# Performance work log

Hardware: AMD Instinct MI355X
Metric: run time of the kernel (lower is better)

## Reference

```python
import jax, jax.numpy as jnp
import numpy as np
from jax import lax

B, L, D, F, K = 16, 1024, 384, 1536, 3
MAX_DUR = 10          # clamp on per-token duration (makes output length static)
T_OUT = L * MAX_DUR   # padded expanded length
ALPHA = 1.0
EPS = 1e-5


def conv1d_same(x_ncl, w, b):
    # x_ncl: [B, Cin, L], w: [Cout, Cin, K]
    y = lax.conv_general_dilated(x_ncl, w, window_strides=(1,), padding='SAME',
                                 dimension_numbers=('NCH', 'OIH', 'NCH'))
    return y + b[None, :, None]


def conv_block(x, wA, bA, wB, bB):
    # x: [B, L, D] -> Conv(D->F) ReLU Conv(F->D) ReLU -> [B, L, D]
    h = x.transpose(0, 2, 1)
    h = jax.nn.relu(conv1d_same(h, wA, bA))
    h = jax.nn.relu(conv1d_same(h, wB, bB))
    return h.transpose(0, 2, 1)


def layernorm(x, g, b):
    mu = jnp.mean(x, axis=-1, keepdims=True)
    var = jnp.var(x, axis=-1, keepdims=True)
    return (x - mu) * lax.rsqrt(var + EPS) * g + b


def setup_inputs() -> dict:
    key = jax.random.key(0)
    ks = jax.random.split(key, 8)
    s = 0.02
    return {
        'y': jax.random.normal(ks[0], (B, L, D), jnp.float32),
        'token_lengths': jax.random.randint(ks[1], (B,), 1, L + 1).astype(jnp.int32),
        'w1a': jax.random.normal(ks[2], (F, D, K), jnp.float32) * s,
        'b1a': jnp.zeros((F,), jnp.float32),
        'w1b': jax.random.normal(ks[3], (D, F, K), jnp.float32) * s,
        'b1b': jnp.zeros((D,), jnp.float32),
        'g1': jnp.ones((D,), jnp.float32),
        'be1': jnp.zeros((D,), jnp.float32),
        'w2a': jax.random.normal(ks[4], (F, D, K), jnp.float32) * s,
        'b2a': jnp.zeros((F,), jnp.float32),
        'w2b': jax.random.normal(ks[5], (D, F, K), jnp.float32) * s,
        'b2b': jnp.zeros((D,), jnp.float32),
        'g2': jnp.ones((D,), jnp.float32),
        'be2': jnp.zeros((D,), jnp.float32),
        'wl': jax.random.normal(ks[6], (D, 1), jnp.float32) * s,
        'bl': jnp.zeros((1,), jnp.float32),
    }


def reference(y, token_lengths, w1a, b1a, w1b, b1b, g1, be1,
              w2a, b2a, w2b, b2b, g2, be2, wl, bl):
    # DurationPredictor (eval mode: dropout is identity)
    h = conv_block(y, w1a, b1a, w1b, b1b)
    h = layernorm(h, g1, be1)
    h = conv_block(h, w2a, b2a, w2b, b2b)
    h = layernorm(h, g2, be2)
    preds = h @ wl + bl                      # [B, L, 1]

    # lengths = round(alpha * exp(preds)), masked to valid tokens, clamped
    lns = jnp.round(ALPHA * jnp.exp(preds[..., 0]))
    lns = jnp.clip(lns, 0, MAX_DUR).astype(jnp.int32)        # [B, L]
    mask = jnp.arange(L)[None, :] < token_lengths[:, None]
    lns = jnp.where(mask, lns, 0)

    # ragged repeat_interleave + pad, fully vectorized:
    # output frame t maps to token idx = searchsorted(cumsum(lns), t, 'right')
    csum = jnp.cumsum(lns, axis=1)                            # [B, L]
    totals = csum[:, -1]                                      # [B]
    t = jnp.arange(T_OUT, dtype=jnp.int32)
    idx = jax.vmap(lambda c: jnp.searchsorted(c, t, side='right'))(csum)  # [B, T_OUT]
    idx = jnp.minimum(idx, L - 1)
    gathered = jnp.take_along_axis(y, idx[..., None], axis=1)  # [B, T_OUT, D]
    valid = t[None, :] < totals[:, None]
    enlarged = jnp.where(valid[..., None], gathered, 0.0)
    return enlarged, totals
```

## Files before the change

### kernel.cpp

```cpp
#include <hip/hip_runtime.h>
#include <hip/hip_bf16.h>

#define BB 16
#define LL 1024
#define DD 384
#define FF 1536
#define KK 3
#define T_OUT 10240
#define MAX_DUR 10

#define PADL 1026
#define LO_SCALE 2048.0f
#define LO_INV   4.8828125e-4f

typedef _Float16 f16x8 __attribute__((ext_vector_type(8)));
typedef float    f32x4 __attribute__((ext_vector_type(4)));

__device__ __forceinline__ void gll16(const void* g, void* l) {
    __builtin_amdgcn_global_load_lds(
        (const __attribute__((address_space(1))) void*)g,
        (__attribute__((address_space(3))) void*)l, 16, 0, 0);
}

__device__ __forceinline__ void split_write(float v, _Float16* hi, _Float16* lo, size_t off) {
    _Float16 h = (_Float16)v;
    hi[off] = h;
    lo[off] = (_Float16)((v - (float)h) * LO_SCALE);
}

__device__ __forceinline__ float split_read(const _Float16* hi, const _Float16* lo, size_t off) {
    return (float)hi[off] + (float)lo[off] * LO_INV;
}

__global__ void wfrag_k(const float* __restrict__ w, _Float16* __restrict__ hi,
                        _Float16* __restrict__ lo, int O, int I) {
    int id = blockIdx.x * 256 + threadIdx.x;
    int total = O * 3 * I;
    if (id >= total) return;
    int e = id & 7;
    int lane = (id >> 3) & 63;
    int rest = id >> 9;
    int nKT = (3 * I) >> 5;
    int ktl = rest % nKT;
    int ot = rest / nKT;
    int o = ot * 16 + (lane & 15);
    int koff = ((lane >> 4) << 3) + e;
    int kseg = ktl % 3;
    int i = (ktl / 3) * 32 + koff;
    float v = w[(o * I + i) * 3 + kseg];
    split_write(v, hi, lo, id);
}

__global__ void ysplit_k(const float* __restrict__ y, _Float16* __restrict__ hi,
                         _Float16* __restrict__ lo) {
    int id = blockIdx.x * 256 + threadIdx.x;
    if (id >= BB * PADL * DD) return;
    int d = id % DD;
    int r = id / DD;
    int b = r / PADL;
    int lr = r - b * PADL;
    float v = 0.f;
    if (lr >= 1 && lr <= LL) v = y[((size_t)(b << 10) + (lr - 1)) * DD + d];
    split_write(v, hi, lo, id);
}

__global__ void padzero_k(_Float16* __restrict__ hi, _Float16* __restrict__ lo, int width) {
    int id = blockIdx.x * 256 + threadIdx.x;
    if (id >= BB * 2 * width) return;
    int b = id / (2 * width);
    int rem = id - b * 2 * width;
    int row = (rem / width) ? (PADL - 1) : 0;
    int c = rem % width;
    size_t off = (size_t)(b * PADL + row) * width + c;
    hi[off] = (_Float16)0.f;
    lo[off] = (_Float16)0.f;
}

__global__ __launch_bounds__(256, 2) void gemm_split(
        const _Float16* __restrict__ Ahi, const _Float16* __restrict__ Alo,
        const _Float16* __restrict__ WfH, const _Float16* __restrict__ WfL,
        const float* __restrict__ bias,
        _Float16* __restrict__ Ohi, _Float16* __restrict__ Olo,
        int Cin, int Cout, int Ktot, int nN) {
    __shared__ _Float16 lds_h[16384];
    const int tid = threadIdx.x;
    const int lane = tid & 63;
    const int w = tid >> 6;
    const int lm = lane & 15, lq = lane >> 4;
    const int xcd = blockIdx.x & 7;
    const int t2 = blockIdx.x >> 3;
    const int g  = t2 / (4 * nN);
    const int r  = t2 - g * (4 * nN);
    const int n_t = r >> 2;
    const int mi  = r & 3;
    const int m_t = ((g * 4 + mi) << 3) + xcd;
    const int m0 = m_t << 7;
    const int n0 = n_t << 7;
    const int b = m0 >> 10;
    const int l0 = m0 & 1023;
    const int rowBase = b * PADL + l0;
    const int wm = (w >> 1) * 64, wn = (w & 1) * 64;

    f32x4 accM[4][4], accC[4][4];
    const f32x4 zz = {0.f, 0.f, 0.f, 0.f};
    #pragma unroll
    for (int i = 0; i < 4; ++i)
        #pragma unroll
        for (int jj = 0; jj < 4; ++jj) { accM[i][jj] = zz; accC[i][jj] = zz; }

    const int nKT = Ktot >> 5;

    auto stageA = [&](int kt, int nxt) {
        int kseg = kt % 3;
        int d0 = (kt / 3) << 5;
        #pragma unroll
        for (int it = 0; it < 2; ++it) {
            int s = (w * 2 + it) * 64 + lane;
            int p = s >> 3, sl = s & 7;
            int t = sl ^ (p & 7);
            int m = p * 2 + (t >> 2);
            int k8 = t & 3;
            size_t aoff = (size_t)(rowBase + m + kseg) * Cin + d0 + k8 * 8;
            _Float16* lbase = lds_h + nxt * 8192 + (size_t)(w * 2 + it) * 512;
            gll16(Ahi + aoff, lbase);
            gll16(Alo + aoff, lbase + 4096);
        }
    };

    auto loadB = [&](int kt, f16x8* bH, f16x8* bL) {
        int ktc = kt < nKT ? kt : nKT - 1;
        #pragma unroll
        for (int jj = 0; jj < 4; ++jj) {
            int ntg = (n0 + wn + jj * 16) >> 4;
            size_t boff = (((size_t)ntg * nKT + ktc) * 64 + lane) * 8;
            bH[jj] = *(const f16x8*)(WfH + boff);
            bL[jj] = *(const f16x8*)(WfL + boff);
        }
    };

    auto compute = [&](const _Float16* lb, const f16x8* bH, const f16x8* bL) {
        #pragma unroll
        for (int i = 0; i < 4; ++i) {
            int m = wm + i * 16 + lm;
            int p = m >> 1;
            int sl = (((m & 1) << 2) | lq) ^ (p & 7);
            int off = p * 64 + sl * 8;
            f16x8 aH = *(const f16x8*)(lb + off);
            f16x8 aL = *(const f16x8*)(lb + 4096 + off);
            #pragma unroll
            for (int jj = 0; jj < 4; ++jj) {
                accM[i][jj] = __builtin_amdgcn_mfma_f32_16x16x32_f16(aH, bH[jj], accM[i][jj], 0, 0, 0);
                accC[i][jj] = __builtin_amdgcn_mfma_f32_16x16x32_f16(aH, bL[jj], accC[i][jj], 0, 0, 0);
                accC[i][jj] = __builtin_amdgcn_mfma_f32_16x16x32_f16(aL, bH[jj], accC[i][jj], 0, 0, 0);
            }
        }
    };

    f16x8 b0H[4], b0L[4], b1H[4], b1L[4];
    loadB(0, b0H, b0L);
    stageA(0, 0);
    for (int kt = 0; kt < nKT; kt += 2) {
        __syncthreads();
        loadB(kt + 1, b1H, b1L);
        if (kt + 1 < nKT) stageA(kt + 1, 1);
        compute(lds_h, b0H, b0L);
        __syncthreads();
        loadB(kt + 2, b0H, b0L);
        if (kt + 2 < nKT) stageA(kt + 2, 0);
        if (kt + 1 < nKT) compute(lds_h + 8192, b1H, b1L);
    }
    #pragma unroll
    for (int i = 0; i < 4; ++i)
        #pragma unroll
        for (int jj = 0; jj < 4; ++jj) {
            int n_g = n0 + wn + jj * 16 + lm;
            float bv = bias[n_g];
            #pragma unroll
            for (int rr = 0; rr < 4; ++rr) {
                int l = l0 + wm + i * 16 + lq * 4 + rr;
                float v = accM[i][jj][rr] + accC[i][jj][rr] * LO_INV + bv;
                v = fmaxf(v, 0.f);
                size_t off = (size_t)(b * PADL + 1 + l) * Cout + n_g;
                split_write(v, Ohi, Olo, off);
            }
        }
}

__global__ __launch_bounds__(128) void ln_split_k(
        _Float16* __restrict__ hi, _Float16* __restrict__ lo,
        const float* __restrict__ g, const float* __restrict__ be) {
    const int row = blockIdx.x;
    const int b = row >> 10, l = row & 1023;
    const size_t base = (size_t)(b * PADL + 1 + l) * DD;
    const int tid = threadIdx.x;
    float v0 = split_read(hi, lo, base + tid);
    float v1 = split_read(hi, lo, base + tid + 128);
    float v2 = split_read(hi, lo, base + tid + 256);

    __shared__ float sh[2];
    float s = v0 + v1 + v2;
    #pragma unroll
    for (int o = 32; o > 0; o >>= 1) s += __shfl_down(s, o, 64);
    if ((tid & 63) == 0) sh[tid >> 6] = s;
    __syncthreads();
    float mu = (sh[0] + sh[1]) * (1.f / DD);
    __syncthreads();
    float d0 = v0 - mu, d1 = v1 - mu, d2 = v2 - mu;
    float q = d0 * d0 + d1 * d1 + d2 * d2;
    #pragma unroll
    for (int o = 32; o > 0; o >>= 1) q += __shfl_down(q, o, 64);
    if ((tid & 63) == 0) sh[tid >> 6] = q;
    __syncthreads();
    float var = (sh[0] + sh[1]) * (1.f / DD);
    float rs = rsqrtf(var + 1e-5f);
    split_write(d0 * rs * g[tid] + be[tid], hi, lo, base + tid);
    split_write(d1 * rs * g[tid + 128] + be[tid + 128], hi, lo, base + tid + 128);
    split_write(d2 * rs * g[tid + 256] + be[tid + 256], hi, lo, base + tid + 256);
}

__global__ __launch_bounds__(128) void ln_pred_split_k(
        const _Float16* __restrict__ hi, const _Float16* __restrict__ lo,
        const float* __restrict__ g, const float* __restrict__ be,
        const float* __restrict__ wl, const float* __restrict__ bl,
        const int* __restrict__ token_lengths, int* __restrict__ lns) {
    const int row = blockIdx.x;
    const int b = row >> 10, l = row & 1023;
    const size_t base = (size_t)(b * PADL + 1 + l) * DD;
    const int tid = threadIdx.x;
    float v0 = split_read(hi, lo, base + tid);
    float v1 = split_read(hi, lo, base + tid + 128);
    float v2 = split_read(hi, lo, base + tid + 256);

    __shared__ float sh[2];
    float s = v0 + v1 + v2;
    #pragma unroll
    for (int o = 32; o > 0; o >>= 1) s += __shfl_down(s, o, 64);
    if ((tid & 63) == 0) sh[tid >> 6] = s;
    __syncthreads();
    float mu = (sh[0] + sh[1]) * (1.f / DD);
    __syncthreads();
    float d0 = v0 - mu, d1 = v1 - mu, d2 = v2 - mu;
    float q = d0 * d0 + d1 * d1 + d2 * d2;
    #pragma unroll
    for (int o = 32; o > 0; o >>= 1) q += __shfl_down(q, o, 64);
    if ((tid & 63) == 0) sh[tid >> 6] = q;
    __syncthreads();
    float var = (sh[0] + sh[1]) * (1.f / DD);
    float rs = rsqrtf(var + 1e-5f);
    __syncthreads();
    float p = (d0 * rs * g[tid]       + be[tid])       * wl[tid]
            + (d1 * rs * g[tid + 128] + be[tid + 128]) * wl[tid + 128]
            + (d2 * rs * g[tid + 256] + be[tid + 256]) * wl[tid + 256];
    #pragma unroll
    for (int o = 32; o > 0; o >>= 1) p += __shfl_down(p, o, 64);
    if ((tid & 63) == 0) sh[tid >> 6] = p;
    __syncthreads();
    if (tid == 0) {
        float pred = sh[0] + sh[1] + bl[0];
        float e = expf(pred);
        float r = rintf(e);
        r = fminf(fmaxf(r, 0.f), (float)MAX_DUR);
        int v = (int)r;
        if (l >= token_lengths[b]) v = 0;
        lns[row] = v;
    }
}

__global__ __launch_bounds__(1024) void cumsum_k(
        const int* __restrict__ lns, int* __restrict__ csum,
        float* __restrict__ totals_out) {
    __shared__ int s[1024];
    const int b = blockIdx.x, tid = threadIdx.x;
    s[tid] = lns[(b << 10) + tid];
    __syncthreads();
    #pragma unroll
    for (int o = 1; o < 1024; o <<= 1) {
        int t = (tid >= o) ? s[tid - o] : 0;
        __syncthreads();
        s[tid] += t;
        __syncthreads();
    }
    csum[(b << 10) + tid] = s[tid];
    if (tid == 1023) totals_out[b] = (float)s[1023];
}

__global__ __launch_bounds__(256) void gather_k(
        const float* __restrict__ y, const int* __restrict__ csum,
        float* __restrict__ out) {
    int gid = blockIdx.x * 256 + threadIdx.x;
    int c4 = gid % 96;
    int rest = gid / 96;
    int t = rest % T_OUT;
    int b = rest / T_OUT;
    const int* c = csum + (b << 10);
    int total = c[1023];
    float4 r = make_float4(0.f, 0.f, 0.f, 0.f);
    if (t < total) {
        int lo = 0, hi = 1024;
        while (lo < hi) {
            int mid = (lo + hi) >> 1;
            if (c[mid] <= t) lo = mid + 1; else hi = mid;
        }
        int idx = min(lo, LL - 1);
        r = *(const float4*)(y + ((size_t)((b << 10) + idx)) * DD + (c4 << 2));
    }
    *(float4*)(out + ((size_t)b * T_OUT + t) * DD + (c4 << 2)) = r;
}

extern "C" void kernel_launch(void* const* d_in, const int* in_sizes, int n_in,
                              void* d_out, int out_size, void* d_ws, size_t ws_size,
                              hipStream_t stream) {
    const float* y   = (const float*)d_in[0];
    const int*   tok = (const int*)d_in[1];
    const float* w1a = (const float*)d_in[2];
    const float* b1a = (const float*)d_in[3];
    const float* w1b = (const float*)d_in[4];
    const float* b1b = (const float*)d_in[5];
    const float* g1  = (const float*)d_in[6];
    const float* be1 = (const float*)d_in[7];
    const float* w2a = (const float*)d_in[8];
    const float* b2a = (const float*)d_in[9];
    const float* w2b = (const float*)d_in[10];
    const float* b2b = (const float*)d_in[11];
    const float* g2  = (const float*)d_in[12];
    const float* be2 = (const float*)d_in[13];
    const float* wl  = (const float*)d_in[14];
    const float* bl  = (const float*)d_in[15];

    float* out = (float*)d_out;

    const size_t WN   = (size_t)FF * DD * KK;
    const size_t SN   = (size_t)BB * PADL * DD;
    const size_t H1N  = (size_t)BB * PADL * FF;
    _Float16* p = (_Float16*)d_ws;
    _Float16* Wh1a = p;              _Float16* Wl1a = Wh1a + WN;
    _Float16* Wh1b = Wl1a + WN;      _Float16* Wl1b = Wh1b + WN;
    _Float16* Wh2a = Wl1b + WN;      _Float16* Wl2a = Wh2a + WN;
    _Float16* Wh2b = Wl2a + WN;      _Float16* Wl2b = Wh2b + WN;
    _Float16* Shi  = Wl2b + WN;      _Float16* Slo  = Shi + SN;
    _Float16* H1hi = Slo + SN;       _Float16* H1lo = H1hi + H1N;
    int* lns  = (int*)(H1lo + H1N);
    int* csum = lns + BB * LL;

    const int M = BB * LL;

    {
        int n = FF * DD * KK;
        wfrag_k<<<(n + 255) / 256, 256, 0, stream>>>(w1a, Wh1a, Wl1a, FF, DD);
        wfrag_k<<<(n + 255) / 256, 256, 0, stream>>>(w1b, Wh1b, Wl1b, DD, FF);
        wfrag_k<<<(n + 255) / 256, 256, 0, stream>>>(w2a, Wh2a, Wl2a, FF, DD);
        wfrag_k<<<(n + 255) / 256, 256, 0, stream>>>(w2b, Wh2b, Wl2b, DD, FF);
        int ny = BB * PADL * DD;
        ysplit_k<<<(ny + 255) / 256, 256, 0, stream>>>(y, Shi, Slo);
        int np = BB * 2 * FF;
        padzero_k<<<(np + 255) / 256, 256, 0, stream>>>(H1hi, H1lo, FF);
    }
    gemm_split<<<(FF / 128) * (M / 128), 256, 0, stream>>>(Shi, Slo, Wh1a, Wl1a, b1a, H1hi, H1lo, DD, FF, 3 * DD, FF / 128);
    gemm_split<<<(DD / 128) * (M / 128), 256, 0, stream>>>(H1hi, H1lo, Wh1b, Wl1b, b1b, Shi, Slo, FF, DD, 3 * FF, DD / 128);
    ln_split_k<<<M, 128, 0, stream>>>(Shi, Slo, g1, be1);
    gemm_split<<<(FF / 128) * (M / 128), 256, 0, stream>>>(Shi, Slo, Wh2a, Wl2a, b2a, H1hi, H1lo, DD, FF, 3 * DD, FF / 128);
    gemm_split<<<(DD / 128) * (M / 128), 256, 0, stream>>>(H1hi, H1lo, Wh2b, Wl2b, b2b, Shi, Slo, FF, DD, 3 * FF, DD / 128);
    ln_pred_split_k<<<M, 128, 0, stream>>>(Shi, Slo, g2, be2, wl, bl, tok, lns);
    cumsum_k<<<BB, 1024, 0, stream>>>(lns, csum, out + (size_t)BB * T_OUT * DD);
    {
        long long n = (long long)BB * T_OUT * 96;
        gather_k<<<(int)((n + 255) / 256), 256, 0, stream>>>(y, csum, out);
    }
}
```

Measured before the change: 1.072 ms.

## Quad-buffer GEMM A-tiles with vmcnt-based sync and smaller M tile for F->D convs

The split-precision GEMM kernel now uses four LDS stages for the A tiles instead of two. It prefetches two k-steps ahead and waits with an explicit s_waitcnt vmcnt followed by one s_barrier per step, replacing the two __syncthreads per step. It raises wave priority with s_setprio during the MFMA block, and becomes a template over the M tile size. The D-output convs (Cout=384) use a 64-row tile to double their grid, which gives more parallelism on the small-N GEMM. The hardcoded vmcnt value depends on the exact count of outstanding loads and risks a race if the compiler reorders loads.

```diff
diff --git a/kernel.cpp b/kernel.cpp
--- a/kernel.cpp
+++ b/kernel.cpp
@@ -76,13 +76,18 @@
     lo[off] = (_Float16)0.f;
 }
 
+template<int MI>
 __global__ __launch_bounds__(256, 2) void gemm_split(
         const _Float16* __restrict__ Ahi, const _Float16* __restrict__ Alo,
         const _Float16* __restrict__ WfH, const _Float16* __restrict__ WfL,
         const float* __restrict__ bias,
         _Float16* __restrict__ Ohi, _Float16* __restrict__ Olo,
         int Cin, int Cout, int Ktot, int nN) {
-    __shared__ _Float16 lds_h[16384];
+    constexpr int BM   = MI * 32;
+    constexpr int BUFH = MI * 1024;
+    constexpr int NIT  = MI / 2;
+    constexpr int VMK  = 8 + 4 * NIT;
+    __shared__ _Float16 lds_h[8 * BUFH];
     const int tid = threadIdx.x;
     const int lane = tid & 63;
     const int w = tid >> 6;
@@ -94,36 +99,36 @@
     const int n_t = r >> 2;
     const int mi  = r & 3;
     const int m_t = ((g * 4 + mi) << 3) + xcd;
-    const int m0 = m_t << 7;
+    const int m0 = m_t * BM;
     const int n0 = n_t << 7;
     const int b = m0 >> 10;
     const int l0 = m0 & 1023;
     const int rowBase = b * PADL + l0;
-    const int wm = (w >> 1) * 64, wn = (w & 1) * 64;
-
-    f32x4 accM[4][4], accC[4][4];
+    const int wm = (w >> 1) * (MI * 16), wn = (w & 1) * 64;
+
+    f32x4 accM[MI][4], accC[MI][4];
     const f32x4 zz = {0.f, 0.f, 0.f, 0.f};
     #pragma unroll
-    for (int i = 0; i < 4; ++i)
+    for (int i = 0; i < MI; ++i)
         #pragma unroll
         for (int jj = 0; jj < 4; ++jj) { accM[i][jj] = zz; accC[i][jj] = zz; }
 
     const int nKT = Ktot >> 5;
 
-    auto stageA = [&](int kt, int nxt) {
+    auto stageA = [&](int kt, int bidx) {
         int kseg = kt % 3;
         int d0 = (kt / 3) << 5;
         #pragma unroll
-        for (int it = 0; it < 2; ++it) {
-            int s = (w * 2 + it) * 64 + lane;
+        for (int it = 0; it < NIT; ++it) {
+            int s = (w * NIT + it) * 64 + lane;
             int p = s >> 3, sl = s & 7;
             int t = sl ^ (p & 7);
             int m = p * 2 + (t >> 2);
             int k8 = t & 3;
             size_t aoff = (size_t)(rowBase + m + kseg) * Cin + d0 + k8 * 8;
-            _Float16* lbase = lds_h + nxt * 8192 + (size_t)(w * 2 + it) * 512;
+            _Float16* lbase = lds_h + (size_t)bidx * (2 * BUFH) + (size_t)(w * NIT + it) * 512;
             gll16(Ahi + aoff, lbase);
-            gll16(Alo + aoff, lbase + 4096);
+            gll16(Alo + aoff, lbase + BUFH);
         }
     };
 
@@ -139,14 +144,15 @@
     };
 
     auto compute = [&](const _Float16* lb, const f16x8* bH, const f16x8* bL) {
-        #pragma unroll
-        for (int i = 0; i < 4; ++i) {
+        __builtin_amdgcn_s_setprio(1);
+        #pragma unroll
+        for (int i = 0; i < MI; ++i) {
             int m = wm + i * 16 + lm;
             int p = m >> 1;
             int sl = (((m & 1) << 2) | lq) ^ (p & 7);
             int off = p * 64 + sl * 8;
             f16x8 aH = *(const f16x8*)(lb + off);
-            f16x8 aL = *(const f16x8*)(lb + 4096 + off);
+            f16x8 aL = *(const f16x8*)(lb + BUFH + off);
             #pragma unroll
             for (int jj = 0; jj < 4; ++jj) {
                 accM[i][jj] = __builtin_amdgcn_mfma_f32_16x16x32_f16(aH, bH[jj], accM[i][jj], 0, 0, 0);
@@ -154,23 +160,31 @@
                 accC[i][jj] = __builtin_amdgcn_mfma_f32_16x16x32_f16(aL, bH[jj], accC[i][jj], 0, 0, 0);
             }
         }
+        __builtin_amdgcn_s_setprio(0);
     };
 
     f16x8 b0H[4], b0L[4], b1H[4], b1L[4];
+    stageA(0, 0);
     loadB(0, b0H, b0L);
-    stageA(0, 0);
+    stageA(1, 1);
     for (int kt = 0; kt < nKT; kt += 2) {
-        __syncthreads();
         loadB(kt + 1, b1H, b1L);
-        if (kt + 1 < nKT) stageA(kt + 1, 1);
-        compute(lds_h, b0H, b0L);
-        __syncthreads();
+        stageA(kt + 2 < nKT ? kt + 2 : nKT - 1, (kt + 2) & 3);
+        __builtin_amdgcn_sched_barrier(0);
+        asm volatile("s_waitcnt vmcnt(%0)" :: "i"(VMK) : "memory");
+        __builtin_amdgcn_s_barrier();
+        __builtin_amdgcn_sched_barrier(0);
+        compute(lds_h + (size_t)(kt & 3) * (2 * BUFH), b0H, b0L);
         loadB(kt + 2, b0H, b0L);
-        if (kt + 2 < nKT) stageA(kt + 2, 0);
-        if (kt + 1 < nKT) compute(lds_h + 8192, b1H, b1L);
-    }
-    #pragma unroll
-    for (int i = 0; i < 4; ++i)
+        stageA(kt + 3 < nKT ? kt + 3 : nKT - 1, (kt + 3) & 3);
+        __builtin_amdgcn_sched_barrier(0);
+        asm volatile("s_waitcnt vmcnt(%0)" :: "i"(VMK) : "memory");
+        __builtin_amdgcn_s_barrier();
+        __builtin_amdgcn_sched_barrier(0);
+        compute(lds_h + (size_t)((kt + 1) & 3) * (2 * BUFH), b1H, b1L);
+    }
+    #pragma unroll
+    for (int i = 0; i < MI; ++i)
         #pragma unroll
         for (int jj = 0; jj < 4; ++jj) {
             int n_g = n0 + wn + jj * 16 + lm;
@@ -355,11 +369,11 @@
         int np = BB * 2 * FF;
         padzero_k<<<(np + 255) / 256, 256, 0, stream>>>(H1hi, H1lo, FF);
     }
-    gemm_split<<<(FF / 128) * (M / 128), 256, 0, stream>>>(Shi, Slo, Wh1a, Wl1a, b1a, H1hi, H1lo, DD, FF, 3 * DD, FF / 128);
-    gemm_split<<<(DD / 128) * (M / 128), 256, 0, stream>>>(H1hi, H1lo, Wh1b, Wl1b, b1b, Shi, Slo, FF, DD, 3 * FF, DD / 128);
+    gemm_split<4><<<(FF / 128) * (M / 128), 256, 0, stream>>>(Shi, Slo, Wh1a, Wl1a, b1a, H1hi, H1lo, DD, FF, 3 * DD, FF / 128);
+    gemm_split<2><<<(DD / 128) * (M / 64), 256, 0, stream>>>(H1hi, H1lo, Wh1b, Wl1b, b1b, Shi, Slo, FF, DD, 3 * FF, DD / 128);
     ln_split_k<<<M, 128, 0, stream>>>(Shi, Slo, g1, be1);
-    gemm_split<<<(FF / 128) * (M / 128), 256, 0, stream>>>(Shi, Slo, Wh2a, Wl2a, b2a, H1hi, H1lo, DD, FF, 3 * DD, FF / 128);
-    gemm_split<<<(DD / 128) * (M / 128), 256, 0, stream>>>(H1hi, H1lo, Wh2b, Wl2b, b2b, Shi, Slo, FF, DD, 3 * FF, DD / 128);
+    gemm_split<4><<<(FF / 128) * (M / 128), 256, 0, stream>>>(Shi, Slo, Wh2a, Wl2a, b2a, H1hi, H1lo, DD, FF, 3 * DD, FF / 128);
+    gemm_split<2><<<(DD / 128) * (M / 64), 256, 0, stream>>>(H1hi, H1lo, Wh2b, Wl2b, b2b, Shi, Slo, FF, DD, 3 * FF, DD / 128);
     ln_pred_split_k<<<M, 128, 0, stream>>>(Shi, Slo, g2, be2, wl, bl, tok, lns);
     cumsum_k<<<BB, 1024, 0, stream>>>(lns, csum, out + (size_t)BB * T_OUT * DD);
     {
```

Measured after the change: 1.038 ms. 3.2% less time.
